# Kernel optimization log

Hardware: AMD Instinct MI355X
Metric: run time of the kernel (lower is better)

Reference implementation:

```python
import jax, jax.numpy as jnp
import numpy as np
from jax import lax

V, D, H, L, K = 50257, 1024, 2048, 6, 3
B, S = 4, 2048
EPS = 1.1920929e-07  # torch.finfo(float32).eps (torch RMSNorm default eps=None)


def rmsnorm(x, w):
    return x * lax.rsqrt(jnp.mean(x * x, axis=-1, keepdims=True) + EPS) * w


def depthwise_conv(x, w, b):
    # x: (B,S,D), w: (D,1,K) depthwise kernel, padding='same' as in torch Conv1d
    y = lax.conv_general_dilated(x.transpose(0, 2, 1), w, (1,), 'SAME',
                                 dimension_numbers=('NCH', 'OIH', 'NCH'),
                                 feature_group_count=x.shape[-1])
    return y.transpose(0, 2, 1) + b


def mingru(x, h0, wz, bz, wh, bh, wo, bo):
    # minGRU: z=sigmoid(Wz x), h_tilde=Wh x, h_t=(1-z_t)h_{t-1}+z_t h_tilde_t (parallel scan)
    z = jax.nn.sigmoid(jnp.einsum('bsd,hd->bsh', x, wz) + bz)
    htil = jnp.einsum('bsd,hd->bsh', x, wh) + bh
    a, bc = 1.0 - z, z * htil

    def comb(c1, c2):
        a1, b1 = c1
        a2, b2 = c2
        return a1 * a2, a2 * b1 + b2

    A, Bc = lax.associative_scan(comb, (a, bc), axis=1)
    h = A * h0[:, None, :] + Bc                      # (B,S,H)
    out = jnp.einsum('bsh,dh->bsd', h, wo) + bo      # project back to model dim
    return out, h[:, -1]


def setup_inputs():
    key = jax.random.key(0)
    ks = jax.random.split(key, 16)
    sc = 0.02
    p = {}
    p['x'] = jax.random.randint(ks[0], (B, S), 0, V)
    p['h_prev'] = jax.random.normal(ks[1], (B, L, H), jnp.float32)
    p['emb'] = jax.random.normal(ks[2], (V, D), jnp.float32) * sc
    p['conv_dw_w'] = jax.random.normal(ks[3], (L, D, 1, K), jnp.float32) * sc
    p['conv_dw_b'] = jnp.zeros((L, D), jnp.float32)
    p['conv_pw_w'] = jax.random.normal(ks[4], (L, D, D), jnp.float32) * sc
    p['conv_pw_b'] = jnp.zeros((L, D), jnp.float32)
    p['n1_w'] = jnp.ones((L, D), jnp.float32)
    p['wz'] = jax.random.normal(ks[5], (L, H, D), jnp.float32) * sc
    p['bz'] = jnp.zeros((L, H), jnp.float32)
    p['wh'] = jax.random.normal(ks[6], (L, H, D), jnp.float32) * sc
    p['bh'] = jnp.zeros((L, H), jnp.float32)
    p['wo'] = jax.random.normal(ks[7], (L, D, H), jnp.float32) * sc
    p['bo'] = jnp.zeros((L, D), jnp.float32)
    p['n2_w'] = jnp.ones((L, D), jnp.float32)
    p['f1_w'] = jax.random.normal(ks[8], (L, H, D), jnp.float32) * sc
    p['f1_b'] = jnp.zeros((L, H), jnp.float32)
    p['f2_w'] = jax.random.normal(ks[9], (L, D, H), jnp.float32) * sc
    p['f2_b'] = jnp.zeros((L, D), jnp.float32)
    p['norm_w'] = jnp.ones((D,), jnp.float32)
    p['out_w'] = jax.random.normal(ks[10], (H, D), jnp.float32) * sc
    p['out_b'] = jnp.zeros((H,), jnp.float32)
    return p


def reference(x, h_prev, emb, conv_dw_w, conv_dw_b, conv_pw_w, conv_pw_b, n1_w,
              wz, bz, wh, bh, wo, bo, n2_w, f1_w, f1_b, f2_w, f2_b,
              norm_w, out_w, out_b):
    xe = emb[x]                                      # (B,S,D)
    h_next = []
    for l in range(L):
        c = depthwise_conv(xe, conv_dw_w[l], conv_dw_b[l])
        c = jnp.einsum('bsd,ed->bse', c, conv_pw_w[l]) + conv_pw_b[l]  # 1x1 conv
        xe = c + xe
        g, hl = mingru(rmsnorm(xe, n1_w[l]), h_prev[:, l],
                       wz[l], bz[l], wh[l], bh[l], wo[l], bo[l])
        xe = g + xe
        f = rmsnorm(xe, n2_w[l])
        f = jnp.einsum('bsd,hd->bsh', f, f1_w[l]) + f1_b[l]
        f = jax.nn.gelu(f, approximate=False)
        f = jnp.einsum('bsh,dh->bsd', f, f2_w[l]) + f2_b[l]
        xe = f + xe
        h_next.append(hl)
    out = jnp.einsum('bsd,hd->bsh', rmsnorm(xe, norm_w), out_w) + out_b
    return out, jnp.stack(h_next, axis=1)             # (B,S,H), (B,L,H)
```

## Files before the change

kernel.cpp:

```cpp
#include <hip/hip_runtime.h>

typedef __bf16 bf16x8 __attribute__((ext_vector_type(8)));
typedef float f32x4 __attribute__((ext_vector_type(4)));

#define DEVI __device__ __forceinline__

namespace {
constexpr int cB = 4, cS = 2048, cD = 1024, cH = 2048, cL = 6;
constexpr int cM = cB * cS;
constexpr float cEPS = 1.1920929e-07f;
constexpr int NCH = 16, CHS = cS / NCH;
}

DEVI unsigned short f2bf(float f) {
  union { float f; unsigned u; } c; c.f = f;
  const unsigned u = c.u;
  return (unsigned short)((u + 0x7fffu + ((u >> 16) & 1u)) >> 16);
}
DEVI float bf2f(unsigned short h) {
  union { unsigned u; float f; } c; c.u = ((unsigned)h) << 16;
  return c.f;
}

DEVI void gld16(const void* g, void* l) {
  __builtin_amdgcn_global_load_lds(
      (__attribute__((address_space(1))) void*)g,
      (__attribute__((address_space(3))) void*)l, 16, 0, 0);
}

union F4 { float4 v; float a[4]; };

__global__ __launch_bounds__(256) void embed_k(const int* __restrict__ x,
    const float* __restrict__ emb, float* __restrict__ xe) {
  const int bs = blockIdx.x;
  const int idx = x[bs];
  const int t = threadIdx.x;
  *(float4*)&xe[(size_t)bs * cD + t * 4] =
      *(const float4*)&emb[(size_t)idx * cD + t * 4];
}

__global__ __launch_bounds__(256) void dwconv_k(const float* __restrict__ xe,
    const float* __restrict__ w, const float* __restrict__ bias,
    unsigned short* __restrict__ out) {
  const int bs = blockIdx.x;
  const int s = bs & (cS - 1);
  const int t = threadIdx.x;
  const int d = t * 4;
  const size_t base = (size_t)bs * cD + d;
  F4 x0, xm, xp, vb;
  x0.v = *(const float4*)&xe[base];
  xm.v = make_float4(0.f, 0.f, 0.f, 0.f);
  xp.v = make_float4(0.f, 0.f, 0.f, 0.f);
  if (s > 0) xm.v = *(const float4*)&xe[base - cD];
  if (s < cS - 1) xp.v = *(const float4*)&xe[base + cD];
  vb.v = *(const float4*)&bias[d];
  unsigned short o[4];
#pragma unroll
  for (int j = 0; j < 4; ++j) {
    const float w0 = w[(d + j) * 3 + 0];
    const float w1 = w[(d + j) * 3 + 1];
    const float w2 = w[(d + j) * 3 + 2];
    o[j] = f2bf(xm.a[j] * w0 + x0.a[j] * w1 + xp.a[j] * w2 + vb.a[j]);
  }
  *(ushort4*)&out[base] = make_ushort4(o[0], o[1], o[2], o[3]);
}

__global__ __launch_bounds__(256) void rmsnorm_k(const float* __restrict__ x,
    const float* __restrict__ w, unsigned short* __restrict__ o) {
  const int row = blockIdx.x;
  const int t = threadIdx.x;
  const size_t base = (size_t)row * cD + t * 4;
  F4 v; v.v = *(const float4*)&x[base];
  float ss = v.a[0]*v.a[0] + v.a[1]*v.a[1] + v.a[2]*v.a[2] + v.a[3]*v.a[3];
#pragma unroll
  for (int off = 32; off > 0; off >>= 1) ss += __shfl_down(ss, off, 64);
  __shared__ float red[4];
  if ((t & 63) == 0) red[t >> 6] = ss;
  __syncthreads();
  const float scale = rsqrtf((red[0]+red[1]+red[2]+red[3]) * (1.f/cD) + cEPS);
  F4 wv; wv.v = *(const float4*)&w[t * 4];
  *(ushort4*)&o[base] = make_ushort4(
      f2bf(v.a[0]*scale*wv.a[0]), f2bf(v.a[1]*scale*wv.a[1]),
      f2bf(v.a[2]*scale*wv.a[2]), f2bf(v.a[3]*scale*wv.a[3]));
}

__global__ __launch_bounds__(256) void cvt_k(const float* __restrict__ s,
    unsigned short* __restrict__ d, int n) {
  const int i = (blockIdx.x * 256 + threadIdx.x) * 4;
  if (i >= n) return;
  F4 v; v.v = *(const float4*)&s[i];
  *(ushort4*)&d[i] = make_ushort4(f2bf(v.a[0]), f2bf(v.a[1]),
                                  f2bf(v.a[2]), f2bf(v.a[3]));
}

template<int N, int K, int EPI>
__global__ __launch_bounds__(256) void gemm_bt(
    const unsigned short* __restrict__ A, const unsigned short* __restrict__ W,
    const float* __restrict__ bias, float* __restrict__ Cf,
    unsigned short* __restrict__ Cb) {
  __shared__ unsigned short As[128 * 32];
  __shared__ unsigned short Bs[128 * 32];
  const int t = threadIdx.x;
  const int lane = t & 63;
  const int wave = t >> 6;
  const int m0 = blockIdx.x * 128;
  const int n0 = blockIdx.y * 128;
  const int wm = (wave >> 1) * 64;
  const int wn = (wave & 1) * 64;
  const int fr = lane & 15;
  const int fk = (lane >> 4) * 8;

  const int arow = t >> 2;
  const int acol = (t & 3) * 8;
  const unsigned short* gA = A + (size_t)(m0 + arow) * K + acol;
  const unsigned short* gB = W + (size_t)(n0 + arow) * K + acol;
  unsigned short* lA = As + wave * 512;
  unsigned short* lB = Bs + wave * 512;

  f32x4 acc[4][4] = {};
  for (int k0 = 0; k0 < K; k0 += 32) {
    gld16(gA + k0, lA);
    gld16(gA + k0 + (size_t)64 * K, lA + 2048);
    gld16(gB + k0, lB);
    gld16(gB + k0 + (size_t)64 * K, lB + 2048);
    __syncthreads();
    bf16x8 fa[4], fb[4];
#pragma unroll
    for (int i = 0; i < 4; ++i) {
      fa[i] = *(const bf16x8*)&As[(wm + i * 16 + fr) * 32 + fk];
      fb[i] = *(const bf16x8*)&Bs[(wn + i * 16 + fr) * 32 + fk];
    }
#pragma unroll
    for (int i = 0; i < 4; ++i)
#pragma unroll
      for (int j = 0; j < 4; ++j)
        acc[i][j] = __builtin_amdgcn_mfma_f32_16x16x32_bf16(
            fa[i], fb[j], acc[i][j], 0, 0, 0);
    __syncthreads();
  }

  const int r0 = m0 + wm + ((lane >> 4) << 2);
  const int c0 = n0 + wn + fr;
#pragma unroll
  for (int i = 0; i < 4; ++i)
#pragma unroll
    for (int j = 0; j < 4; ++j) {
      const int col = c0 + j * 16;
      const float bv = bias[col];
#pragma unroll
      for (int r = 0; r < 4; ++r) {
        const size_t idx = (size_t)(r0 + i * 16 + r) * N + col;
        const float v = acc[i][j][r] + bv;
        if constexpr (EPI == 1) {
          Cf[idx] += v;
        } else {
          Cf[idx] = v;
        }
      }
    }
}

#define RDA(BUF, MH)                                                        \
  _Pragma("unroll") for (int mf = 0; mf < 4; ++mf)                          \
  _Pragma("unroll") for (int kk = 0; kk < 2; ++kk)                          \
      a[mf * 2 + kk] = *(const bf16x8*)&lds[(BUF)*16384 + aB + (MH)*4096 +  \
                                            mf * 1024 + kk * 32];

#define RDB0(BUF)                                                           \
  _Pragma("unroll") for (int q = 0; q < 2; ++q)                             \
  _Pragma("unroll") for (int kk = 0; kk < 2; ++kk)                          \
      b[0][q * 2 + kk] = *(const bf16x8*)&lds[(BUF)*16384 + bB + q * 1024 + kk * 32];

#define RDB1(BUF)                                                           \
  _Pragma("unroll") for (int q = 2; q < 4; ++q)                             \
  _Pragma("unroll") for (int kk = 0; kk < 2; ++kk)                          \
      b[1][(q & 1) * 2 + kk] =                                              \
          *(const bf16x8*)&lds[(BUF)*16384 + bB + q * 1024 + kk * 32];

#define MMQ(MH, NH)                                                         \
  _Pragma("unroll") for (int mf = 0; mf < 4; ++mf)                          \
  _Pragma("unroll") for (int nf = 0; nf < 2; ++nf)                          \
  _Pragma("unroll") for (int kk = 0; kk < 2; ++kk)                          \
      acc[(MH)*4 + mf][(NH)*2 + nf] = __builtin_amdgcn_mfma_f32_16x16x32_bf16( \
          a[mf * 2 + kk], b[NH][nf * 2 + kk], acc[(MH)*4 + mf][(NH)*2 + nf],  \
          0, 0, 0);

#define PH_SYNC()                                                           \
  __builtin_amdgcn_s_barrier();                                             \
  asm volatile("s_waitcnt lgkmcnt(0)" ::: "memory");                        \
  __builtin_amdgcn_sched_barrier(0);                                        \
  __builtin_amdgcn_s_setprio(1)

#define PH_END()                                                            \
  __builtin_amdgcn_s_setprio(0);                                            \
  __builtin_amdgcn_s_barrier()

#define TILE_PHASES(TI, BUF, OBUF, S1, S2, VM)                              \
  {                                                                         \
    RDA(BUF, 0); RDB0(BUF);                                                 \
    if (S1) { stA((TI) + 1, 1, ldsA(OBUF, 1)); }                            \
    PH_SYNC(); MMQ(0, 0); PH_END();                                         \
    RDB1(BUF);                                                              \
    PH_SYNC(); MMQ(0, 1); PH_END();                                         \
    RDA(BUF, 1);                                                            \
    if (S2) { stB((TI) + 2, 0, ldsB(BUF, 0)); }                             \
    PH_SYNC(); MMQ(1, 1); PH_END();                                         \
    if (S2) { stB((TI) + 2, 1, ldsB(BUF, 1)); stA((TI) + 2, 0, ldsA(BUF, 0)); } \
    if (VM == 6) { asm volatile("s_waitcnt vmcnt(6)" ::: "memory"); }       \
    else         { asm volatile("s_waitcnt vmcnt(0)" ::: "memory"); }       \
    PH_SYNC(); MMQ(1, 0); PH_END();                                         \
  }

template<int N, int K, int EPI, int NS>
__global__ __launch_bounds__(512, 2) void gemm8p(
    const unsigned short* __restrict__ A,
    const unsigned short* __restrict__ W0,
    const unsigned short* __restrict__ W1,
    const float* __restrict__ bias0, const float* __restrict__ bias1,
    float* __restrict__ Cf, unsigned short* __restrict__ Cb,
    unsigned short* __restrict__ Cb2) {
  static_assert(K % 128 == 0, "NT must be even");
  constexpr int NT = K / 64;
  __shared__ unsigned short lds[65536];
  const int t = threadIdx.x;
  const int lane = t & 63;
  const int wave = t >> 6;
  const int wr = wave >> 2;
  const int wc = wave & 3;
  const int m0 = blockIdx.x * 256;
  const int n0 = blockIdx.y * 256;

  const bool zpart = (n0 < NS);
  const unsigned short* Wp = zpart ? W0 : W1;
  const int nw0 = zpart ? n0 : n0 - NS;
  const float* bp = zpart ? bias0 : bias1;
  const int CW = zpart ? NS : (N - NS);

  const int srow = t >> 3;
  const int scol = ((t & 7) * 8) ^ (((t >> 5) & 1) << 4);
  const unsigned short* gA = A  + (size_t)(m0 + srow) * K + scol;
  const unsigned short* gB = Wp + (size_t)(nw0 + srow) * K + scol;
  const int ldsw = wave * 512;

  auto ldsA = [&](int buf, int h) -> unsigned short* {
    return (unsigned short*)&lds[buf * 16384 + h * 8192 + ldsw];
  };
  auto ldsB = [&](int buf, int h) -> unsigned short* {
    return (unsigned short*)&lds[32768 + buf * 16384 + h * 8192 + ldsw];
  };
  auto stA = [&](int tile, int h, unsigned short* dst) {
    const unsigned short* s = gA + (size_t)(h * 128) * K + tile * 64;
    gld16(s, dst);
    gld16(s + (size_t)64 * K, dst + 4096);
  };
  auto stB = [&](int tile, int h, unsigned short* dst) {
    const unsigned short* s = gB + (size_t)(h * 128) * K + tile * 64;
    gld16(s, dst);
    gld16(s + (size_t)64 * K, dst + 4096);
  };

  const int sx = ((lane >> 2) & 1) << 4;
  const int aoff = (lane & 15) * 64 + (((lane >> 4) * 8) ^ sx);
  const int aB = wr * 8192 + aoff;
  const int bB = 32768 + (wc >> 1) * 8192 + (wc & 1) * 4096 + aoff;

  bf16x8 a[8];
  bf16x8 b[2][4];
  f32x4 acc[8][4] = {};

  stA(0, 0, ldsA(0, 0)); stA(0, 1, ldsA(0, 1));
  stB(0, 0, ldsB(0, 0)); stB(0, 1, ldsB(0, 1));
  stA(1, 0, ldsA(1, 0));
  stB(1, 0, ldsB(1, 0)); stB(1, 1, ldsB(1, 1));
  asm volatile("s_waitcnt vmcnt(6)" ::: "memory");
  __builtin_amdgcn_s_barrier();

  for (int tp = 0; tp < NT / 2 - 1; ++tp) {
    const int t0 = 2 * tp;
    TILE_PHASES(t0, 0, 1, 1, 1, 6);
    TILE_PHASES(t0 + 1, 1, 0, 1, 1, 6);
  }
  TILE_PHASES(NT - 2, 0, 1, 1, 0, 0);
  TILE_PHASES(NT - 1, 1, 0, 0, 0, 0);

  const int r0l = wr * 128 + ((lane >> 4) << 2);
  const int c0l = wc * 64 + (lane & 15);
  if constexpr (EPI == 0) {
    const int r0 = m0 + r0l;
    const int c0 = nw0 + c0l;
#pragma unroll
    for (int mfg = 0; mfg < 8; ++mfg)
#pragma unroll
      for (int nfg = 0; nfg < 4; ++nfg) {
        const int col = c0 + nfg * 16;
        const float bv = bp[col];
#pragma unroll
        for (int r = 0; r < 4; ++r)
          Cf[(size_t)(r0 + mfg * 16 + r) * CW + col] = acc[mfg][nfg][r] + bv;
      }
  } else {
    unsigned short* cb = zpart ? Cb : Cb2;
#pragma unroll
    for (int mfg = 0; mfg < 8; ++mfg)
#pragma unroll
      for (int nfg = 0; nfg < 4; ++nfg) {
        const int col = c0l + nfg * 16;
        const float bv = bp[nw0 + col];
#pragma unroll
        for (int r = 0; r < 4; ++r) {
          const float v = acc[mfg][nfg][r] + bv;
          unsigned short o;
          if constexpr (EPI == 4) {
            o = f2bf(0.5f * v * (1.f + erff(v * 0.70710678118654752f)));
          } else {
            o = zpart ? f2bf(1.f / (1.f + __expf(-v))) : f2bf(v);
          }
          const int rr = r0l + mfg * 16 + r;
          lds[rr * 256 + (col ^ (((rr >> 2) & 3) << 4))] = o;
        }
      }
    __syncthreads();
#pragma unroll
    for (int it = 0; it < 16; ++it) {
      const int flat = it * 512 + t;
      const int row = flat >> 5;
      const int ch = flat & 31;
      const float4 v = *(const float4*)&lds[row * 256 + ((ch * 8) ^ (((row >> 2) & 3) << 4))];
      *(float4*)&cb[(size_t)(m0 + row) * CW + nw0 + ch * 8] = v;
    }
  }
}

__global__ __launch_bounds__(256) void scan1_k(const unsigned short* __restrict__ z,
    const unsigned short* __restrict__ ht, float* __restrict__ Ac,
    float* __restrict__ Bc) {
  const int tid = blockIdx.x * 256 + threadIdx.x;
  const int hq = (tid & (cH / 4 - 1)) * 4;
  const int ck = (tid / (cH / 4)) & (NCH - 1);
  const int b = tid / ((cH / 4) * NCH);
  const size_t base = ((size_t)b * cS + (size_t)ck * CHS) * cH + hq;
  float a[4] = {1.f, 1.f, 1.f, 1.f};
  float sb[4] = {0.f, 0.f, 0.f, 0.f};
#pragma unroll 4
  for (int s = 0; s < CHS; ++s) {
    const ushort4 zz = *(const ushort4*)&z[base + (size_t)s * cH];
    const ushort4 hh = *(const ushort4*)&ht[base + (size_t)s * cH];
    const float zf[4] = {bf2f(zz.x), bf2f(zz.y), bf2f(zz.z), bf2f(zz.w)};
    const float hf[4] = {bf2f(hh.x), bf2f(hh.y), bf2f(hh.z), bf2f(hh.w)};
#pragma unroll
    for (int j = 0; j < 4; ++j) {
      const float aa = 1.f - zf[j];
      sb[j] = aa * sb[j] + zf[j] * hf[j];
      a[j] *= aa;
    }
  }
  const size_t so = ((size_t)b * NCH + ck) * cH + hq;
  *(float4*)&Ac[so] = make_float4(a[0], a[1], a[2], a[3]);
  *(float4*)&Bc[so] = make_float4(sb[0], sb[1], sb[2], sb[3]);
}

__global__ __launch_bounds__(256) void scan23_k(const unsigned short* __restrict__ z,
    unsigned short* __restrict__ ht, const float* __restrict__ Ac,
    const float* __restrict__ Bc, const float* __restrict__ h_prev,
    float* __restrict__ hn, int l) {
  const int tid = blockIdx.x * 256 + threadIdx.x;
  const int hq = (tid & (cH / 4 - 1)) * 4;
  const int ck = (tid / (cH / 4)) & (NCH - 1);
  const int b = tid / ((cH / 4) * NCH);
  const size_t hoff = ((size_t)b * cL + l) * cH + hq;
  F4 h0; h0.v = *(const float4*)&h_prev[hoff];
  float r[4] = {h0.a[0], h0.a[1], h0.a[2], h0.a[3]};
  for (int c = 0; c < ck; ++c) {
    const size_t so = ((size_t)b * NCH + c) * cH + hq;
    F4 av, bv;
    av.v = *(const float4*)&Ac[so];
    bv.v = *(const float4*)&Bc[so];
#pragma unroll
    for (int j = 0; j < 4; ++j) r[j] = av.a[j] * r[j] + bv.a[j];
  }
  const size_t base = ((size_t)b * cS + (size_t)ck * CHS) * cH + hq;
#pragma unroll 4
  for (int s = 0; s < CHS; ++s) {
    const ushort4 zz = *(const ushort4*)&z[base + (size_t)s * cH];
    const ushort4 hh = *(const ushort4*)&ht[base + (size_t)s * cH];
    const float zf[4] = {bf2f(zz.x), bf2f(zz.y), bf2f(zz.z), bf2f(zz.w)};
    const float hf[4] = {bf2f(hh.x), bf2f(hh.y), bf2f(hh.z), bf2f(hh.w)};
#pragma unroll
    for (int j = 0; j < 4; ++j) r[j] = (1.f - zf[j]) * r[j] + zf[j] * hf[j];
    *(ushort4*)&ht[base + (size_t)s * cH] =
        make_ushort4(f2bf(r[0]), f2bf(r[1]), f2bf(r[2]), f2bf(r[3]));
  }
  if (ck == NCH - 1)
    *(float4*)&hn[hoff] = make_float4(r[0], r[1], r[2], r[3]);
}

extern "C" void kernel_launch(void* const* d_in, const int* in_sizes, int n_in,
                              void* d_out, int out_size, void* d_ws, size_t ws_size,
                              hipStream_t stream) {
  (void)in_sizes; (void)n_in; (void)out_size; (void)ws_size;
  const int*   x      = (const int*)d_in[0];
  const float* h_prev = (const float*)d_in[1];
  const float* emb    = (const float*)d_in[2];
  const float* cdw_w  = (const float*)d_in[3];
  const float* cdw_b  = (const float*)d_in[4];
  const float* cpw_w  = (const float*)d_in[5];
  const float* cpw_b  = (const float*)d_in[6];
  const float* n1w    = (const float*)d_in[7];
  const float* wzp    = (const float*)d_in[8];
  const float* bzp    = (const float*)d_in[9];
  const float* whp    = (const float*)d_in[10];
  const float* bhp    = (const float*)d_in[11];
  const float* wop    = (const float*)d_in[12];
  const float* bop    = (const float*)d_in[13];
  const float* n2w    = (const float*)d_in[14];
  const float* f1wp   = (const float*)d_in[15];
  const float* f1bp   = (const float*)d_in[16];
  const float* f2wp   = (const float*)d_in[17];
  const float* f2bp   = (const float*)d_in[18];
  const float* nw     = (const float*)d_in[19];
  const float* owp    = (const float*)d_in[20];
  const float* obp    = (const float*)d_in[21];

  float* out_main = (float*)d_out;
  float* out_hn   = out_main + (size_t)cM * cH;

  char* p = (char*)d_ws;
  auto alloc = [&](size_t bytes) {
    char* r = p; p += (bytes + 255) & ~(size_t)255; return r;
  };
  float*          xe = (float*)alloc((size_t)cM * cD * 4);
  unsigned short* xn = (unsigned short*)alloc((size_t)cM * cD * 2);
  unsigned short* zb = (unsigned short*)alloc((size_t)cM * cH * 2);
  unsigned short* hb = (unsigned short*)alloc((size_t)cM * cH * 2);
  float* Ac = (float*)alloc((size_t)cB * NCH * cH * 4);
  float* Bc = (float*)alloc((size_t)cB * NCH * cH * 4);
  unsigned short* w_pw = (unsigned short*)alloc((size_t)cL * cD * cD * 2);
  unsigned short* w_z  = (unsigned short*)alloc((size_t)cL * cH * cD * 2);
  unsigned short* w_h  = (unsigned short*)alloc((size_t)cL * cH * cD * 2);
  unsigned short* w_o  = (unsigned short*)alloc((size_t)cL * cD * cH * 2);
  unsigned short* w_f1 = (unsigned short*)alloc((size_t)cL * cH * cD * 2);
  unsigned short* w_f2 = (unsigned short*)alloc((size_t)cL * cD * cH * 2);
  unsigned short* w_ow = (unsigned short*)alloc((size_t)cH * cD * 2);

  auto cvt = [&](const float* src, unsigned short* dst, size_t n) {
    cvt_k<<<dim3((unsigned)(n / 1024)), 256, 0, stream>>>(src, dst, (int)n);
  };

  cvt(cpw_w, w_pw, (size_t)cL * cD * cD);
  cvt(wzp,  w_z,  (size_t)cL * cH * cD);
  cvt(whp,  w_h,  (size_t)cL * cH * cD);
  cvt(wop,  w_o,  (size_t)cL * cD * cH);
  cvt(f1wp, w_f1, (size_t)cL * cH * cD);
  cvt(f2wp, w_f2, (size_t)cL * cD * cH);
  cvt(owp,  w_ow, (size_t)cH * cD);

  embed_k<<<cM, 256, 0, stream>>>(x, emb, xe);

  for (int l = 0; l < cL; ++l) {
    const size_t oDD = (size_t)l * cD * cD, oHD = (size_t)l * cH * cD;

    dwconv_k<<<cM, 256, 0, stream>>>(xe, cdw_w + (size_t)l * cD * 3,
                                     cdw_b + (size_t)l * cD, xn);
    gemm_bt<cD, cD, 1><<<dim3(cM / 128, cD / 128), 256, 0, stream>>>(
        xn, w_pw + oDD, cpw_b + (size_t)l * cD, xe, nullptr);

    rmsnorm_k<<<cM, 256, 0, stream>>>(xe, n1w + (size_t)l * cD, xn);
    gemm8p<2 * cH, cD, 5, cH><<<dim3(cM / 256, 2 * cH / 256), 512, 0, stream>>>(
        xn, w_z + oHD, w_h + oHD, bzp + (size_t)l * cH, bhp + (size_t)l * cH,
        nullptr, zb, hb);
    scan1_k<<<cB * NCH * (cH / 4) / 256, 256, 0, stream>>>(zb, hb, Ac, Bc);
    scan23_k<<<cB * NCH * (cH / 4) / 256, 256, 0, stream>>>(zb, hb, Ac, Bc,
                                                            h_prev, out_hn, l);
    gemm_bt<cD, cH, 1><<<dim3(cM / 128, cD / 128), 256, 0, stream>>>(
        hb, w_o + oHD, bop + (size_t)l * cD, xe, nullptr);

    rmsnorm_k<<<cM, 256, 0, stream>>>(xe, n2w + (size_t)l * cD, xn);
    gemm8p<cH, cD, 4, cH><<<dim3(cM / 256, cH / 256), 512, 0, stream>>>(
        xn, w_f1 + oHD, w_f1 + oHD, f1bp + (size_t)l * cH, f1bp + (size_t)l * cH,
        nullptr, zb, zb);
    gemm_bt<cD, cH, 1><<<dim3(cM / 128, cD / 128), 256, 0, stream>>>(
        zb, w_f2 + oHD, f2bp + (size_t)l * cD, xe, nullptr);
  }

  rmsnorm_k<<<cM, 256, 0, stream>>>(xe, nw, xn);
  gemm8p<cH, cD, 0, cH><<<dim3(cM / 256, cH / 256), 512, 0, stream>>>(
      xn, w_ow, w_ow, obp, obp, out_main, nullptr, nullptr);
}
```

Baseline: 2.415 ms.

## Interleave z/h weights and fuse chunk scan into the z/h GEMM epilogue

The Wz and Wh weights and biases are interleaved row-wise so each GEMM tile produces paired z and h columns. The epilogue de-interleaves them into separate z and h buffers and, while the tile is still in LDS, computes the per-chunk scan products (A, B) for 128-step chunks. This removes the separate scan1 kernel and its re-read of z and h from global memory. The cost is extra serial epilogue work done by only half the threads, plus two extra interleave kernels at setup.

```diff
diff --git a/kernel.cpp b/kernel.cpp
--- a/kernel.cpp
+++ b/kernel.cpp
@@ -93,6 +93,27 @@
                                   f2bf(v.a[2]), f2bf(v.a[3]));
 }
 
+template<int WHICH>
+__global__ __launch_bounds__(256) void cvti_k(const float* __restrict__ s,
+    unsigned short* __restrict__ d) {
+  const size_t i = ((size_t)blockIdx.x * 256 + threadIdx.x) * 4;
+  const int l = (int)(i >> 21);
+  const int r = (int)((i >> 10) & (cH - 1));
+  const int c = (int)(i & (cD - 1));
+  F4 v; v.v = *(const float4*)&s[i];
+  const size_t di = (((size_t)l * 2 * cH) + 2 * r + WHICH) * cD + c;
+  *(ushort4*)&d[di] = make_ushort4(f2bf(v.a[0]), f2bf(v.a[1]),
+                                   f2bf(v.a[2]), f2bf(v.a[3]));
+}
+
+template<int WHICH>
+__global__ __launch_bounds__(256) void biasi_k(const float* __restrict__ s,
+    float* __restrict__ d) {
+  const int i = blockIdx.x * 256 + threadIdx.x;
+  const int l = i >> 11, h = i & (cH - 1);
+  d[((size_t)l * 2 * cH) + 2 * h + WHICH] = s[i];
+}
+
 template<int N, int K, int EPI>
 __global__ __launch_bounds__(256) void gemm_bt(
     const unsigned short* __restrict__ A, const unsigned short* __restrict__ W,
@@ -211,14 +232,14 @@
     PH_SYNC(); MMQ(1, 0); PH_END();                                         \
   }
 
-template<int N, int K, int EPI, int NS>
+template<int N, int K, int EPI>
 __global__ __launch_bounds__(512, 2) void gemm8p(
     const unsigned short* __restrict__ A,
     const unsigned short* __restrict__ W0,
-    const unsigned short* __restrict__ W1,
-    const float* __restrict__ bias0, const float* __restrict__ bias1,
+    const float* __restrict__ bias0,
     float* __restrict__ Cf, unsigned short* __restrict__ Cb,
-    unsigned short* __restrict__ Cb2) {
+    unsigned short* __restrict__ Cb2,
+    float* __restrict__ Ac, float* __restrict__ Bc) {
   static_assert(K % 128 == 0, "NT must be even");
   constexpr int NT = K / 64;
   __shared__ unsigned short lds[65536];
@@ -230,16 +251,10 @@
   const int m0 = blockIdx.x * 256;
   const int n0 = blockIdx.y * 256;
 
-  const bool zpart = (n0 < NS);
-  const unsigned short* Wp = zpart ? W0 : W1;
-  const int nw0 = zpart ? n0 : n0 - NS;
-  const float* bp = zpart ? bias0 : bias1;
-  const int CW = zpart ? NS : (N - NS);
-
   const int srow = t >> 3;
   const int scol = ((t & 7) * 8) ^ (((t >> 5) & 1) << 4);
   const unsigned short* gA = A  + (size_t)(m0 + srow) * K + scol;
-  const unsigned short* gB = Wp + (size_t)(nw0 + srow) * K + scol;
+  const unsigned short* gB = W0 + (size_t)(n0 + srow) * K + scol;
   const int ldsw = wave * 512;
 
   auto ldsA = [&](int buf, int h) -> unsigned short* {
@@ -287,25 +302,25 @@
   const int c0l = wc * 64 + (lane & 15);
   if constexpr (EPI == 0) {
     const int r0 = m0 + r0l;
-    const int c0 = nw0 + c0l;
+    const int c0 = n0 + c0l;
 #pragma unroll
     for (int mfg = 0; mfg < 8; ++mfg)
 #pragma unroll
       for (int nfg = 0; nfg < 4; ++nfg) {
         const int col = c0 + nfg * 16;
-        const float bv = bp[col];
+        const float bv = bias0[col];
 #pragma unroll
         for (int r = 0; r < 4; ++r)
-          Cf[(size_t)(r0 + mfg * 16 + r) * CW + col] = acc[mfg][nfg][r] + bv;
+          Cf[(size_t)(r0 + mfg * 16 + r) * N + col] = acc[mfg][nfg][r] + bv;
       }
   } else {
-    unsigned short* cb = zpart ? Cb : Cb2;
+    const bool isz = ((lane & 1) == 0);
 #pragma unroll
     for (int mfg = 0; mfg < 8; ++mfg)
 #pragma unroll
       for (int nfg = 0; nfg < 4; ++nfg) {
         const int col = c0l + nfg * 16;
-        const float bv = bp[nw0 + col];
+        const float bv = bias0[n0 + col];
 #pragma unroll
         for (int r = 0; r < 4; ++r) {
           const float v = acc[mfg][nfg][r] + bv;
@@ -313,50 +328,65 @@
           if constexpr (EPI == 4) {
             o = f2bf(0.5f * v * (1.f + erff(v * 0.70710678118654752f)));
           } else {
-            o = zpart ? f2bf(1.f / (1.f + __expf(-v))) : f2bf(v);
+            o = isz ? f2bf(1.f / (1.f + __expf(-v))) : f2bf(v);
           }
           const int rr = r0l + mfg * 16 + r;
           lds[rr * 256 + (col ^ (((rr >> 2) & 3) << 4))] = o;
         }
       }
     __syncthreads();
-#pragma unroll
-    for (int it = 0; it < 16; ++it) {
-      const int flat = it * 512 + t;
-      const int row = flat >> 5;
-      const int ch = flat & 31;
-      const float4 v = *(const float4*)&lds[row * 256 + ((ch * 8) ^ (((row >> 2) & 3) << 4))];
-      *(float4*)&cb[(size_t)(m0 + row) * CW + nw0 + ch * 8] = v;
+    if constexpr (EPI == 4) {
+#pragma unroll
+      for (int it = 0; it < 16; ++it) {
+        const int flat = it * 512 + t;
+        const int row = flat >> 5;
+        const int ch = flat & 31;
+        const float4 v = *(const float4*)&lds[row * 256 +
+                                              ((ch * 8) ^ (((row >> 2) & 3) << 4))];
+        *(float4*)&Cb[(size_t)(m0 + row) * N + n0 + ch * 8] = v;
+      }
+    } else {
+#pragma unroll
+      for (int it = 0; it < 16; ++it) {
+        const int flat = it * 512 + t;
+        const int row = flat >> 5;
+        const int ch = flat & 31;
+        union { float4 v; unsigned u[4]; } q;
+        q.v = *(const float4*)&lds[row * 256 +
+                                   ((ch * 8) ^ (((row >> 2) & 3) << 4))];
+        const ushort4 zz = make_ushort4(q.u[0] & 0xffff, q.u[1] & 0xffff,
+                                        q.u[2] & 0xffff, q.u[3] & 0xffff);
+        const ushort4 hh = make_ushort4(q.u[0] >> 16, q.u[1] >> 16,
+                                        q.u[2] >> 16, q.u[3] >> 16);
+        const size_t o = (size_t)(m0 + row) * (N / 2) + (n0 >> 1) + ch * 4;
+        *(ushort4*)&Cb[o]  = zz;
+        *(ushort4*)&Cb2[o] = hh;
+      }
+      if (t < 256) {
+        const int lc = t >> 7;
+        const int lh = t & 127;
+        float av = 1.f, bv = 0.f;
+        const int s0 = lc * 128;
+#pragma unroll 4
+        for (int s = 0; s < CHS; ++s) {
+          const int sr = s0 + s;
+          const int c = (2 * lh) ^ (((sr >> 2) & 3) << 4);
+          const unsigned w2 = *(const unsigned*)&lds[sr * 256 + c];
+          const float zv = bf2f((unsigned short)(w2 & 0xffff));
+          const float hv = bf2f((unsigned short)(w2 >> 16));
+          const float aa = 1.f - zv;
+          bv = aa * bv + zv * hv;
+          av *= aa;
+        }
+        const int bidx = m0 / cS;
+        const int ck = ((m0 & (cS - 1)) >> 7) + lc;
+        const int hg = (n0 >> 1) + lh;
+        const size_t so = ((size_t)bidx * NCH + ck) * cH + hg;
+        Ac[so] = av;
+        Bc[so] = bv;
+      }
     }
   }
-}
-
-__global__ __launch_bounds__(256) void scan1_k(const unsigned short* __restrict__ z,
-    const unsigned short* __restrict__ ht, float* __restrict__ Ac,
-    float* __restrict__ Bc) {
-  const int tid = blockIdx.x * 256 + threadIdx.x;
-  const int hq = (tid & (cH / 4 - 1)) * 4;
-  const int ck = (tid / (cH / 4)) & (NCH - 1);
-  const int b = tid / ((cH / 4) * NCH);
-  const size_t base = ((size_t)b * cS + (size_t)ck * CHS) * cH + hq;
-  float a[4] = {1.f, 1.f, 1.f, 1.f};
-  float sb[4] = {0.f, 0.f, 0.f, 0.f};
-#pragma unroll 4
-  for (int s = 0; s < CHS; ++s) {
-    const ushort4 zz = *(const ushort4*)&z[base + (size_t)s * cH];
-    const ushort4 hh = *(const ushort4*)&ht[base + (size_t)s * cH];
-    const float zf[4] = {bf2f(zz.x), bf2f(zz.y), bf2f(zz.z), bf2f(zz.w)};
-    const float hf[4] = {bf2f(hh.x), bf2f(hh.y), bf2f(hh.z), bf2f(hh.w)};
-#pragma unroll
-    for (int j = 0; j < 4; ++j) {
-      const float aa = 1.f - zf[j];
-      sb[j] = aa * sb[j] + zf[j] * hf[j];
-      a[j] *= aa;
-    }
-  }
-  const size_t so = ((size_t)b * NCH + ck) * cH + hq;
-  *(float4*)&Ac[so] = make_float4(a[0], a[1], a[2], a[3]);
-  *(float4*)&Bc[so] = make_float4(sb[0], sb[1], sb[2], sb[3]);
 }
 
 __global__ __launch_bounds__(256) void scan23_k(const unsigned short* __restrict__ z,
@@ -435,8 +465,8 @@
   float* Ac = (float*)alloc((size_t)cB * NCH * cH * 4);
   float* Bc = (float*)alloc((size_t)cB * NCH * cH * 4);
   unsigned short* w_pw = (unsigned short*)alloc((size_t)cL * cD * cD * 2);
-  unsigned short* w_z  = (unsigned short*)alloc((size_t)cL * cH * cD * 2);
-  unsigned short* w_h  = (unsigned short*)alloc((size_t)cL * cH * cD * 2);
+  unsigned short* w_zh = (unsigned short*)alloc((size_t)cL * 2 * cH * cD * 2);
+  float*          bzh  = (float*)alloc((size_t)cL * 2 * cH * 4);
   unsigned short* w_o  = (unsigned short*)alloc((size_t)cL * cD * cH * 2);
   unsigned short* w_f1 = (unsigned short*)alloc((size_t)cL * cH * cD * 2);
   unsigned short* w_f2 = (unsigned short*)alloc((size_t)cL * cD * cH * 2);
@@ -447,8 +477,10 @@
   };
 
   cvt(cpw_w, w_pw, (size_t)cL * cD * cD);
-  cvt(wzp,  w_z,  (size_t)cL * cH * cD);
-  cvt(whp,  w_h,  (size_t)cL * cH * cD);
+  cvti_k<0><<<dim3(cL * cH * cD / 1024), 256, 0, stream>>>(wzp, w_zh);
+  cvti_k<1><<<dim3(cL * cH * cD / 1024), 256, 0, stream>>>(whp, w_zh);
+  biasi_k<0><<<dim3(cL * cH / 256), 256, 0, stream>>>(bzp, bzh);
+  biasi_k<1><<<dim3(cL * cH / 256), 256, 0, stream>>>(bhp, bzh);
   cvt(wop,  w_o,  (size_t)cL * cD * cH);
   cvt(f1wp, w_f1, (size_t)cL * cH * cD);
   cvt(f2wp, w_f2, (size_t)cL * cD * cH);
@@ -465,24 +497,23 @@
         xn, w_pw + oDD, cpw_b + (size_t)l * cD, xe, nullptr);
 
     rmsnorm_k<<<cM, 256, 0, stream>>>(xe, n1w + (size_t)l * cD, xn);
-    gemm8p<2 * cH, cD, 5, cH><<<dim3(cM / 256, 2 * cH / 256), 512, 0, stream>>>(
-        xn, w_z + oHD, w_h + oHD, bzp + (size_t)l * cH, bhp + (size_t)l * cH,
-        nullptr, zb, hb);
-    scan1_k<<<cB * NCH * (cH / 4) / 256, 256, 0, stream>>>(zb, hb, Ac, Bc);
+    gemm8p<2 * cH, cD, 6><<<dim3(cM / 256, 2 * cH / 256), 512, 0, stream>>>(
+        xn, w_zh + (size_t)l * 2 * cH * cD, bzh + (size_t)l * 2 * cH,
+        nullptr, zb, hb, Ac, Bc);
     scan23_k<<<cB * NCH * (cH / 4) / 256, 256, 0, stream>>>(zb, hb, Ac, Bc,
                                                             h_prev, out_hn, l);
     gemm_bt<cD, cH, 1><<<dim3(cM / 128, cD / 128), 256, 0, stream>>>(
         hb, w_o + oHD, bop + (size_t)l * cD, xe, nullptr);
 
     rmsnorm_k<<<cM, 256, 0, stream>>>(xe, n2w + (size_t)l * cD, xn);
-    gemm8p<cH, cD, 4, cH><<<dim3(cM / 256, cH / 256), 512, 0, stream>>>(
-        xn, w_f1 + oHD, w_f1 + oHD, f1bp + (size_t)l * cH, f1bp + (size_t)l * cH,
-        nullptr, zb, zb);
+    gemm8p<cH, cD, 4><<<dim3(cM / 256, cH / 256), 512, 0, stream>>>(
+        xn, w_f1 + oHD, f1bp + (size_t)l * cH, nullptr, zb, nullptr,
+        nullptr, nullptr);
     gemm_bt<cD, cH, 1><<<dim3(cM / 128, cD / 128), 256, 0, stream>>>(
         zb, w_f2 + oHD, f2bp + (size_t)l * cD, xe, nullptr);
   }
 
   rmsnorm_k<<<cM, 256, 0, stream>>>(xe, nw, xn);
-  gemm8p<cH, cD, 0, cH><<<dim3(cM / 256, cH / 256), 512, 0, stream>>>(
-      xn, w_ow, w_ow, obp, obp, out_main, nullptr, nullptr);
-}
+  gemm8p<cH, cD, 0><<<dim3(cM / 256, cH / 256), 512, 0, stream>>>(
+      xn, w_ow, obp, out_main, nullptr, nullptr, nullptr, nullptr);
+}
```

New measurement: 2.384 ms. About the same (-1.3%).
